# Kernel tuning notes

Hardware: AMD Instinct MI355X
Metric: run time of the kernel (lower is better)

Reference implementation:

```python
import jax, jax.numpy as jnp
import numpy as np

D_MODEL = 1024
HEADS = 8
WINDOW = 64
N_PATCH = 512
N_TOK = 512
TEXT_D = 768
IMAGE_D = 1024
B = 1


def _sliding_window_attn(x, ctx, qw, qb, kw, kb, vw, vb, ow, ob, window, heads):
    # Faithful to the torch loop: window i covers context[max(0,i-w//2) : min(T,i+w//2+1)+1],
    # i.e. up to w+2 real tokens; zero-padded (unmasked!) up to w tokens when shorter.
    B_, N, Dm = x.shape
    T = ctx.shape[1]
    L = window + 2
    dh = Dm // heads
    q = x @ qw.T + qb  # (B,N,D)
    idx = jnp.arange(N)[:, None] + (jnp.arange(L) - window // 2)[None, :]  # (N,L)
    valid = (idx >= 0) & (idx < T)                      # real context tokens
    length = valid.sum(-1)                              # real tokens per window
    n_zero = jnp.maximum(0, window - length)            # zero-pad count (torch pads to w)
    inv_rank = jnp.cumsum(~valid, axis=-1) - 1          # rank among invalid slots
    attend = valid | ((~valid) & (inv_rank < n_zero[:, None]))  # real + zero-pad slots
    ctxw = jnp.where(valid[None, :, :, None], ctx[:, jnp.clip(idx, 0, T - 1), :], 0.0)  # (B,N,L,D)
    k = ctxw @ kw.T + kb                                # bias hits zero-pad slots too (as torch)
    v = ctxw @ vw.T + vb
    qh = q.reshape(B_, N, heads, dh)
    kh = k.reshape(B_, N, L, heads, dh)
    vh = v.reshape(B_, N, L, heads, dh)
    s = jnp.einsum('bnhd,bnlhd->bhnl', qh, kh) / jnp.sqrt(jnp.asarray(dh, x.dtype))
    s = jnp.where(attend[None, None], s, jnp.asarray(-1e9, x.dtype))
    a = jax.nn.softmax(s, axis=-1)
    o = jnp.einsum('bhnl,bnlhd->bnhd', a, vh).reshape(B_, N, Dm)
    return o @ ow.T + ob + x  # residual add, as in torch loop


def setup_inputs() -> dict:
    key = jax.random.key(0)
    ks = jax.random.split(key, 32)
    s = 0.02
    inp = {
        'images': jax.random.normal(ks[0], (B, N_PATCH, IMAGE_D), jnp.float32),
        'capitions': jax.random.normal(ks[1], (B, N_TOK, TEXT_D), jnp.float32),
        'text_input_ids': jax.random.randint(ks[2], (B, N_TOK), 0, 32000, jnp.int64)
        if jax.config.jax_enable_x64 else jax.random.randint(ks[2], (B, N_TOK), 0, 32000, jnp.int32),
        'tp_w': jax.random.normal(ks[3], (D_MODEL, TEXT_D), jnp.float32) * s,
        'tp_b': jnp.zeros((D_MODEL,), jnp.float32),
        'ip_w': jax.random.normal(ks[4], (D_MODEL, IMAGE_D), jnp.float32) * s,
        'ip_b': jnp.zeros((D_MODEL,), jnp.float32),
    }
    names = ['qw', 'kw', 'vw', 'ow']
    i = 5
    for pre in ['ia_', 'ta_']:
        for n in names:
            inp[pre + n] = jax.random.normal(ks[i], (D_MODEL, D_MODEL), jnp.float32) * s
            inp[pre + n[0] + 'b'] = jnp.zeros((D_MODEL,), jnp.float32)
            i += 1
    return inp


def reference(images, capitions, text_input_ids,
              tp_w, tp_b, ip_w, ip_b,
              ia_qw, ia_qb, ia_kw, ia_kb, ia_vw, ia_vb, ia_ow, ia_ob,
              ta_qw, ta_qb, ta_kw, ta_kb, ta_vw, ta_vb, ta_ow, ta_ob):
    txt = capitions @ tp_w.T + tp_b   # (B,Ntok,D)
    img = images @ ip_w.T + ip_b      # (B,Npatch,D)
    fused_img = _sliding_window_attn(img, txt, ia_qw, ia_qb, ia_kw, ia_kb,
                                     ia_vw, ia_vb, ia_ow, ia_ob, WINDOW, HEADS)
    fused_txt = _sliding_window_attn(txt, img, ta_qw, ta_qb, ta_kw, ta_kb,
                                     ta_vw, ta_vb, ta_ow, ta_ob, WINDOW, HEADS)
    return fused_img, fused_txt
```

## Files before the change

kernel.cpp:

```cpp
#include <hip/hip_runtime.h>
#include <hip/hip_bf16.h>

#define MDIM 512
#define NDIM 1024
#define LSLOT 66

typedef __attribute__((ext_vector_type(8))) short short8;
typedef __attribute__((ext_vector_type(4))) short short4v;
typedef __attribute__((ext_vector_type(4))) float f32x4;
typedef __hip_bfloat16 bf16;

static __device__ __forceinline__ short f2bf(float f) {
    return __builtin_bit_cast(short, __float2bfloat16(f));
}
static __device__ __forceinline__ short8 cvt8(float4 a, float4 b) {
    short8 v;
    v[0] = f2bf(a.x); v[1] = f2bf(a.y); v[2] = f2bf(a.z); v[3] = f2bf(a.w);
    v[4] = f2bf(b.x); v[5] = f2bf(b.y); v[6] = f2bf(b.z); v[7] = f2bf(b.w);
    return v;
}

static __device__ __forceinline__ void gload16(const void* g, void* l) {
    __builtin_amdgcn_global_load_lds(
        (const __attribute__((address_space(1))) unsigned int*)g,
        (__attribute__((address_space(3))) unsigned int*)l, 16, 0, 0);
}

struct CvtDesc { const float* src; bf16* dst; int n; };
struct CvtBatch { CvtDesc d[12]; };

__global__ __launch_bounds__(256) void cvt_bf16(CvtBatch cb) {
    CvtDesc c = cb.d[blockIdx.z];
    const int i = (blockIdx.x * 256 + threadIdx.x) * 8;
    if (i >= c.n) return;
    const float4 a = *(const float4*)(c.src + i);
    const float4 b = *(const float4*)(c.src + i + 4);
    *(short8*)((short*)c.dst + i) = cvt8(a, b);
}

struct GDesc {
    const bf16* A;
    const bf16* W;
    const float* bias;
    const float* res;
    float* C;
    bf16* Cb;
    int K;
};
struct GBatch { GDesc d[6]; };

__global__ __launch_bounds__(128) void gemm_bf16(GBatch gb) {
    GDesc g = gb.d[blockIdx.z];
    const int K = g.K;
    __shared__ __align__(16) short lds[3][2][64 * 64];

    const int tid  = threadIdx.x;
    const int lane = tid & 63;
    const int wave = tid >> 6;
    const int m0 = blockIdx.y * 64;
    const int n0 = blockIdx.x * 64;
    const int wm = wave * 32;

    const size_t rowb = (size_t)K * 2;
    const char* sbase = (const char*)(wave ? (const void*)g.W : (const void*)g.A)
                      + (size_t)(wave ? n0 : m0) * rowb
                      + (size_t)(lane >> 3) * rowb
                      + (size_t)(((lane & 7) ^ (lane >> 3)) << 4);

    const int fr = lane & 15;
    const int fq = lane >> 4;

    f32x4 acc[2][4] = {};
    const int NT = K / 64;

#pragma unroll
    for (int tt = 0; tt < 3; ++tt)
#pragma unroll
        for (int i = 0; i < 8; ++i)
            gload16(sbase + (size_t)tt * 128 + (size_t)i * 8 * rowb,
                    &lds[tt][wave][i * 512]);

#define GSTEP(VMW)                                                              \
    {                                                                           \
        asm volatile("s_waitcnt vmcnt(" #VMW ")" ::: "memory");                 \
        __builtin_amdgcn_s_barrier();         \
        __builtin_amdgcn_sched_barrier(0);                                      \
        const int b = t % 3;                                                    \
        short8 af[2][2], wf[4][2];                                              \
        _Pragma("unroll")                                                       \
        for (int kk = 0; kk < 2; ++kk) {                                        \
            const int ch = kk * 4 + fq;                                         \
            _Pragma("unroll")                                                   \
            for (int i = 0; i < 2; ++i) {                                       \
                const int r = wm + i * 16 + fr;                                 \
                af[i][kk] = *(const short8*)&lds[b][0][r * 64 + ((ch ^ (r & 7)) << 3)]; \
            }                                                                   \
            _Pragma("unroll")                                                   \
            for (int j = 0; j < 4; ++j) {                                       \
                const int c = j * 16 + fr;                                      \
                wf[j][kk] = *(const short8*)&lds[b][1][c * 64 + ((ch ^ (c & 7)) << 3)]; \
            }                                                                   \
        }                                                                       \
        asm volatile("s_waitcnt lgkmcnt(0)" ::: "memory");                      \
        __builtin_amdgcn_sched_barrier(0);                                      \
        __builtin_amdgcn_s_barrier();              \
        if (t + 3 < NT) {                                                       \
            const char* p = sbase + (size_t)(t + 3) * 128;                      \
            _Pragma("unroll")                                                   \
            for (int i = 0; i < 8; ++i)                                         \
                gload16(p + (size_t)i * 8 * rowb, &lds[b][wave][i * 512]);      \
        }                                                                       \
        _Pragma("unroll")                                                       \
        for (int kk = 0; kk < 2; ++kk)                                          \
            _Pragma("unroll")                                                   \
            for (int i = 0; i < 2; ++i)                                         \
                _Pragma("unroll")                                               \
                for (int j = 0; j < 4; ++j)                                     \
                    acc[i][j] = __builtin_amdgcn_mfma_f32_16x16x32_bf16(        \
                        af[i][kk], wf[j][kk], acc[i][j], 0, 0, 0);              \
    }

    int t = 0;
    for (; t < NT - 2; ++t) GSTEP(16)
    GSTEP(8)
    ++t;
    GSTEP(0)
#undef GSTEP

#pragma unroll
    for (int i = 0; i < 2; ++i) {
        const int row0 = m0 + wm + i * 16 + fq * 4;
#pragma unroll
        for (int j = 0; j < 4; ++j) {
            const int col = n0 + j * 16 + fr;
            const float b = g.bias[col];
#pragma unroll
            for (int r = 0; r < 4; ++r) {
                float v = acc[i][j][r] + b;
                const size_t o = (size_t)(row0 + r) * NDIM + col;
                if (g.res) v += g.res[o];
                g.C[o] = v;
                if (g.Cb) g.Cb[o] = __float2bfloat16(v);
            }
        }
    }
}

struct AttnArgs {
    const float *Q, *K, *V, *kb, *vb;
    bf16* O;
};

__global__ __launch_bounds__(256) void attn_tile(AttnArgs a0, AttnArgs a1) {
    const AttnArgs a = blockIdx.z ? a1 : a0;
    const int h  = blockIdx.y;
    const int n0 = blockIdx.x * 32;
    const int tid = threadIdx.x;

    __shared__ float Ks[97 * 128];
    __shared__ float Vs[97 * 128];
    __shared__ float Qs[32 * 132];
    __shared__ float Ps[32 * 68];
    __shared__ float InvS[32];

    for (int i = tid; i < 97 * 32; i += 256) {
        const int wp = i >> 5, d4 = i & 31;
        const int idx = n0 - 32 + wp;
        const bool valid = (idx >= 0) && (idx < MDIM);
        const float* sk = (valid ? (a.K + (size_t)idx * NDIM) : a.kb) + h * 128;
        const float* sv = (valid ? (a.V + (size_t)idx * NDIM) : a.vb) + h * 128;
        const float4 kv = *(const float4*)(sk + d4 * 4);
        const float4 vv = *(const float4*)(sv + d4 * 4);
        const int slot = d4 ^ (wp & 31);
        *(float4*)&Ks[wp * 128 + slot * 4] = kv;
        *(float4*)&Vs[wp * 128 + slot * 4] = vv;
    }
    for (int i = tid; i < 32 * 32; i += 256) {
        const int r = i >> 5, d4 = i & 31;
        *(float4*)&Qs[r * 132 + d4 * 4] =
            *(const float4*)(a.Q + (size_t)(n0 + r) * NDIM + h * 128 + d4 * 4);
    }
    __syncthreads();

    const int r = tid >> 3, sub = tid & 7;
    const int n = n0 + r;
    const int lo_inv = max(0, 32 - n);
    const int hi_inv = max(0, n - 478);
    const int n_zero = max(0, 64 - (LSLOT - lo_inv - hi_inv));
    const float scale = 0.088388347648318447f;

    float dots[9];
#pragma unroll
    for (int k = 0; k < 9; ++k) dots[k] = 0.f;
#pragma unroll
    for (int db = 0; db < 4; ++db) {
        float4 q[8];
#pragma unroll
        for (int c = 0; c < 8; ++c) q[c] = *(float4*)&Qs[r * 132 + (db * 8 + c) * 4];
        for (int k = 0; k < 9; ++k) {
            const int l = sub + 8 * k;
            if (l >= LSLOT) break;
            const int wp = r + l, key = wp & 31;
            float accd = dots[k];
#pragma unroll
            for (int c = 0; c < 8; ++c) {
                const int d4 = db * 8 + c;
                const float4 kv = *(float4*)&Ks[wp * 128 + (d4 ^ key) * 4];
                accd += kv.x * q[c].x + kv.y * q[c].y + kv.z * q[c].z + kv.w * q[c].w;
            }
            dots[k] = accd;
        }
    }
    for (int k = 0; k < 9; ++k) {
        const int l = sub + 8 * k;
        if (l >= LSLOT) break;
        const int idx = n - 32 + l;
        const bool valid = (idx >= 0) && (idx < MDIM);
        bool attend = valid;
        if (!valid) {
            const int ir = (l < lo_inv) ? l : (l - (LSLOT - hi_inv));
            attend = ir < n_zero;
        }
        Ps[r * 68 + l] = attend ? dots[k] * scale : -1e30f;
    }
    __syncthreads();

    {
        float m = -1e30f;
        for (int k = 0; k < 9; ++k) {
            const int l = sub + 8 * k;
            if (l < LSLOT) m = fmaxf(m, Ps[r * 68 + l]);
        }
        for (int s = 1; s < 8; s <<= 1) m = fmaxf(m, __shfl_xor(m, s, 64));
        float sum = 0.f;
        for (int k = 0; k < 9; ++k) {
            const int l = sub + 8 * k;
            if (l >= LSLOT) break;
            const float e = expf(Ps[r * 68 + l] - m);
            Ps[r * 68 + l] = e;
            sum += e;
        }
        for (int s = 1; s < 8; s <<= 1) sum += __shfl_xor(sum, s, 64);
        if (sub == 0) InvS[r] = 1.0f / sum;
    }
    __syncthreads();

    float4 acc[4] = {};
    for (int l = 0; l < LSLOT; ++l) {
        const float p = Ps[r * 68 + l];
        const int wp = r + l, key = wp & 31;
#pragma unroll
        for (int c = 0; c < 4; ++c) {
            const int d4 = sub + 8 * c;
            const float4 vv = *(float4*)&Vs[wp * 128 + (d4 ^ key) * 4];
            acc[c].x += p * vv.x; acc[c].y += p * vv.y;
            acc[c].z += p * vv.z; acc[c].w += p * vv.w;
        }
    }
    const float inv = InvS[r];
#pragma unroll
    for (int c = 0; c < 4; ++c) {
        short4v o;
        o[0] = f2bf(acc[c].x * inv); o[1] = f2bf(acc[c].y * inv);
        o[2] = f2bf(acc[c].z * inv); o[3] = f2bf(acc[c].w * inv);
        *(short4v*)((short*)a.O + (size_t)n * NDIM + h * 128 + (sub + 8 * c) * 4) = o;
    }
}

extern "C" void kernel_launch(void* const* d_in, const int* in_sizes, int n_in,
                              void* d_out, int out_size, void* d_ws, size_t ws_size,
                              hipStream_t stream) {
    const float* images = (const float*)d_in[0];
    const float* caps   = (const float*)d_in[1];
    const float* tp_w = (const float*)d_in[3];
    const float* tp_b = (const float*)d_in[4];
    const float* ip_w = (const float*)d_in[5];
    const float* ip_b = (const float*)d_in[6];
    const float* ia_qw = (const float*)d_in[7];  const float* ia_qb = (const float*)d_in[8];
    const float* ia_kw = (const float*)d_in[9];  const float* ia_kb = (const float*)d_in[10];
    const float* ia_vw = (const float*)d_in[11]; const float* ia_vb = (const float*)d_in[12];
    const float* ia_ow = (const float*)d_in[13]; const float* ia_ob = (const float*)d_in[14];
    const float* ta_qw = (const float*)d_in[15]; const float* ta_qb = (const float*)d_in[16];
    const float* ta_kw = (const float*)d_in[17]; const float* ta_kb = (const float*)d_in[18];
    const float* ta_vw = (const float*)d_in[19]; const float* ta_vb = (const float*)d_in[20];
    const float* ta_ow = (const float*)d_in[21]; const float* ta_ob = (const float*)d_in[22];

    const size_t S = (size_t)MDIM * NDIM;
    float* ws = (float*)d_ws;
    float* txt = ws + 0 * S;
    float* img = ws + 1 * S;
    float* Qi  = ws + 2 * S;
    float* Ki  = ws + 3 * S;
    float* Vi  = ws + 4 * S;
    float* Qt  = ws + 5 * S;
    float* Kt  = ws + 6 * S;
    float* Vt  = ws + 7 * S;
    bf16* bb     = (bf16*)(ws + 8 * S);
    bf16* capsb  = bb;
    bf16* imgsb  = capsb + 393216;
    bf16* txtb   = imgsb + S;
    bf16* imgb   = txtb + S;
    bf16* Oib    = imgb + S;
    bf16* Otb    = Oib + S;
    bf16* tp_wb  = Otb + S;
    bf16* ip_wb  = tp_wb + 786432;
    bf16* qwb[8];
    { bf16* p = ip_wb + 1048576;
      for (int i = 0; i < 8; ++i) { qwb[i] = p; p += 1048576; } }

    float* fused_img = (float*)d_out;
    float* fused_txt = (float*)d_out + S;

    CvtBatch cv = {};
    cv.d[0]  = {caps,   capsb, 393216};
    cv.d[1]  = {images, imgsb, (int)S};
    cv.d[2]  = {tp_w,   tp_wb, 786432};
    cv.d[3]  = {ip_w,   ip_wb, 1048576};
    cv.d[4]  = {ia_qw, qwb[0], 1048576};
    cv.d[5]  = {ia_kw, qwb[1], 1048576};
    cv.d[6]  = {ia_vw, qwb[2], 1048576};
    cv.d[7]  = {ia_ow, qwb[3], 1048576};
    cv.d[8]  = {ta_qw, qwb[4], 1048576};
    cv.d[9]  = {ta_kw, qwb[5], 1048576};
    cv.d[10] = {ta_vw, qwb[6], 1048576};
    cv.d[11] = {ta_ow, qwb[7], 1048576};
    cvt_bf16<<<dim3(512, 1, 12), 256, 0, stream>>>(cv);

    dim3 blk(128);
    dim3 tiles(NDIM / 64, MDIM / 64);

    GBatch b1 = {};
    b1.d[0] = {capsb, tp_wb, tp_b, nullptr, txt, txtb, 768};
    b1.d[1] = {imgsb, ip_wb, ip_b, nullptr, img, imgb, 1024};
    gemm_bf16<<<dim3(tiles.x, tiles.y, 2), blk, 0, stream>>>(b1);

    GBatch b2 = {};
    b2.d[0] = {imgb, qwb[0], ia_qb, nullptr, Qi, nullptr, 1024};
    b2.d[1] = {txtb, qwb[1], ia_kb, nullptr, Ki, nullptr, 1024};
    b2.d[2] = {txtb, qwb[2], ia_vb, nullptr, Vi, nullptr, 1024};
    b2.d[3] = {txtb, qwb[4], ta_qb, nullptr, Qt, nullptr, 1024};
    b2.d[4] = {imgb, qwb[5], ta_kb, nullptr, Kt, nullptr, 1024};
    b2.d[5] = {imgb, qwb[6], ta_vb, nullptr, Vt, nullptr, 1024};
    gemm_bf16<<<dim3(tiles.x, tiles.y, 6), blk, 0, stream>>>(b2);

    AttnArgs aa = {Qi, Ki, Vi, ia_kb, ia_vb, Oib};
    AttnArgs ab = {Qt, Kt, Vt, ta_kb, ta_vb, Otb};
    attn_tile<<<dim3(16, 8, 2), 256, 0, stream>>>(aa, ab);

    GBatch b4 = {};
    b4.d[0] = {Oib, qwb[3], ia_ob, img, fused_img, nullptr, 1024};
    b4.d[1] = {Otb, qwb[7], ta_ob, txt, fused_txt, nullptr, 1024};
    gemm_bf16<<<dim3(tiles.x, tiles.y, 2), blk, 0, stream>>>(b4);
}
```

Before: 179.8 us.

## Fuse all stages into one persistent kernel with atomic grid barriers

Merges the bf16 conversion, the projection GEMMs, the QKV GEMMs, the attention and the output GEMM into a single 256-block kernel. Stages are separated by software grid barriers built on atomic counters, which are zeroed with a memset before each launch. Each block runs two GEMM tile units of two waves each, and the attention stage reuses the same shared memory. The aim is to remove four kernel launch gaps and tail effects. In exchange it relies on all 256 blocks being resident at once, uses large LDS per block, and leaves some blocks idle in stages with fewer tiles.

```diff
diff --git a/kernel.cpp b/kernel.cpp
--- a/kernel.cpp
+++ b/kernel.cpp
@@ -4,6 +4,7 @@
 #define MDIM 512
 #define NDIM 1024
 #define LSLOT 66
+#define NBLK 256u
 
 typedef __attribute__((ext_vector_type(8))) short short8;
 typedef __attribute__((ext_vector_type(4))) short short4v;
@@ -19,7 +20,6 @@
     v[4] = f2bf(b.x); v[5] = f2bf(b.y); v[6] = f2bf(b.z); v[7] = f2bf(b.w);
     return v;
 }
-
 static __device__ __forceinline__ void gload16(const void* g, void* l) {
     __builtin_amdgcn_global_load_lds(
         (const __attribute__((address_space(1))) unsigned int*)g,
@@ -27,17 +27,6 @@
 }
 
 struct CvtDesc { const float* src; bf16* dst; int n; };
-struct CvtBatch { CvtDesc d[12]; };
-
-__global__ __launch_bounds__(256) void cvt_bf16(CvtBatch cb) {
-    CvtDesc c = cb.d[blockIdx.z];
-    const int i = (blockIdx.x * 256 + threadIdx.x) * 8;
-    if (i >= c.n) return;
-    const float4 a = *(const float4*)(c.src + i);
-    const float4 b = *(const float4*)(c.src + i + 4);
-    *(short8*)((short*)c.dst + i) = cvt8(a, b);
-}
-
 struct GDesc {
     const bf16* A;
     const bf16* W;
@@ -47,28 +36,38 @@
     bf16* Cb;
     int K;
 };
-struct GBatch { GDesc d[6]; };
-
-__global__ __launch_bounds__(128) void gemm_bf16(GBatch gb) {
-    GDesc g = gb.d[blockIdx.z];
+struct AttnArgs { const float *Q, *K, *V, *kb, *vb; bf16* O; };
+struct FusedArgs {
+    CvtDesc cv[12];
+    GDesc s1[2], s2[6], s4[2];
+    AttnArgs at[2];
+    unsigned* bar;
+};
+
+static __device__ __forceinline__ void grid_bar(unsigned* ctr) {
+    __syncthreads();
+    if (threadIdx.x == 0) {
+        __threadfence();
+        __hip_atomic_fetch_add(ctr, 1u, __ATOMIC_ACQ_REL, __HIP_MEMORY_SCOPE_AGENT);
+        while (__hip_atomic_load(ctr, __ATOMIC_ACQUIRE, __HIP_MEMORY_SCOPE_AGENT) < NBLK)
+            __builtin_amdgcn_s_sleep(4);
+        __threadfence();
+    }
+    __syncthreads();
+}
+
+static __device__ void gemm_tile(const GDesc& g, int m0, int n0,
+                                 short* L, int w2, int lane) {
     const int K = g.K;
-    __shared__ __align__(16) short lds[3][2][64 * 64];
-
-    const int tid  = threadIdx.x;
-    const int lane = tid & 63;
-    const int wave = tid >> 6;
-    const int m0 = blockIdx.y * 64;
-    const int n0 = blockIdx.x * 64;
-    const int wm = wave * 32;
-
     const size_t rowb = (size_t)K * 2;
-    const char* sbase = (const char*)(wave ? (const void*)g.W : (const void*)g.A)
-                      + (size_t)(wave ? n0 : m0) * rowb
+    const char* sbase = (const char*)(w2 ? (const void*)g.W : (const void*)g.A)
+                      + (size_t)(w2 ? n0 : m0) * rowb
                       + (size_t)(lane >> 3) * rowb
                       + (size_t)(((lane & 7) ^ (lane >> 3)) << 4);
-
     const int fr = lane & 15;
     const int fq = lane >> 4;
+    const int wm = w2 * 32;
+    short* Lw = L + w2 * 4096;
 
     f32x4 acc[2][4] = {};
     const int NT = K / 64;
@@ -78,12 +77,12 @@
 #pragma unroll
         for (int i = 0; i < 8; ++i)
             gload16(sbase + (size_t)tt * 128 + (size_t)i * 8 * rowb,
-                    &lds[tt][wave][i * 512]);
+                    Lw + tt * 8192 + i * 512);
 
 #define GSTEP(VMW)                                                              \
     {                                                                           \
         asm volatile("s_waitcnt vmcnt(" #VMW ")" ::: "memory");                 \
-        __builtin_amdgcn_s_barrier();         \
+        __builtin_amdgcn_s_barrier();          \
         __builtin_amdgcn_sched_barrier(0);                                      \
         const int b = t % 3;                                                    \
         short8 af[2][2], wf[4][2];                                              \
@@ -93,12 +92,12 @@
             _Pragma("unroll")                                                   \
             for (int i = 0; i < 2; ++i) {                                       \
                 const int r = wm + i * 16 + fr;                                 \
-                af[i][kk] = *(const short8*)&lds[b][0][r * 64 + ((ch ^ (r & 7)) << 3)]; \
+                af[i][kk] = *(const short8*)&L[b * 8192 + r * 64 + ((ch ^ (r & 7)) << 3)]; \
             }                                                                   \
             _Pragma("unroll")                                                   \
             for (int j = 0; j < 4; ++j) {                                       \
                 const int c = j * 16 + fr;                                      \
-                wf[j][kk] = *(const short8*)&lds[b][1][c * 64 + ((ch ^ (c & 7)) << 3)]; \
+                wf[j][kk] = *(const short8*)&L[b * 8192 + 4096 + c * 64 + ((ch ^ (c & 7)) << 3)]; \
             }                                                                   \
         }                                                                       \
         asm volatile("s_waitcnt lgkmcnt(0)" ::: "memory");                      \
@@ -108,7 +107,7 @@
             const char* p = sbase + (size_t)(t + 3) * 128;                      \
             _Pragma("unroll")                                                   \
             for (int i = 0; i < 8; ++i)                                         \
-                gload16(p + (size_t)i * 8 * rowb, &lds[b][wave][i * 512]);      \
+                gload16(p + (size_t)i * 8 * rowb, Lw + b * 8192 + i * 512);     \
         }                                                                       \
         _Pragma("unroll")                                                       \
         for (int kk = 0; kk < 2; ++kk)                                          \
@@ -146,124 +145,173 @@
     }
 }
 
-struct AttnArgs {
-    const float *Q, *K, *V, *kb, *vb;
-    bf16* O;
-};
-
-__global__ __launch_bounds__(256) void attn_tile(AttnArgs a0, AttnArgs a1) {
-    const AttnArgs a = blockIdx.z ? a1 : a0;
-    const int h  = blockIdx.y;
-    const int n0 = blockIdx.x * 32;
-    const int tid = threadIdx.x;
-
-    __shared__ float Ks[97 * 128];
-    __shared__ float Vs[97 * 128];
-    __shared__ float Qs[32 * 132];
-    __shared__ float Ps[32 * 68];
-    __shared__ float InvS[32];
-
-    for (int i = tid; i < 97 * 32; i += 256) {
-        const int wp = i >> 5, d4 = i & 31;
-        const int idx = n0 - 32 + wp;
-        const bool valid = (idx >= 0) && (idx < MDIM);
-        const float* sk = (valid ? (a.K + (size_t)idx * NDIM) : a.kb) + h * 128;
-        const float* sv = (valid ? (a.V + (size_t)idx * NDIM) : a.vb) + h * 128;
-        const float4 kv = *(const float4*)(sk + d4 * 4);
-        const float4 vv = *(const float4*)(sv + d4 * 4);
-        const int slot = d4 ^ (wp & 31);
-        *(float4*)&Ks[wp * 128 + slot * 4] = kv;
-        *(float4*)&Vs[wp * 128 + slot * 4] = vv;
-    }
-    for (int i = tid; i < 32 * 32; i += 256) {
-        const int r = i >> 5, d4 = i & 31;
-        *(float4*)&Qs[r * 132 + d4 * 4] =
-            *(const float4*)(a.Q + (size_t)(n0 + r) * NDIM + h * 128 + d4 * 4);
-    }
-    __syncthreads();
-
-    const int r = tid >> 3, sub = tid & 7;
-    const int n = n0 + r;
-    const int lo_inv = max(0, 32 - n);
-    const int hi_inv = max(0, n - 478);
-    const int n_zero = max(0, 64 - (LSLOT - lo_inv - hi_inv));
-    const float scale = 0.088388347648318447f;
-
-    float dots[9];
-#pragma unroll
-    for (int k = 0; k < 9; ++k) dots[k] = 0.f;
-#pragma unroll
-    for (int db = 0; db < 4; ++db) {
-        float4 q[8];
-#pragma unroll
-        for (int c = 0; c < 8; ++c) q[c] = *(float4*)&Qs[r * 132 + (db * 8 + c) * 4];
+__global__ __launch_bounds__(256) void fused(FusedArgs fa) {
+    __shared__ __align__(16) char smem[125056];
+    const int tid  = threadIdx.x;
+    const int bi   = blockIdx.x;
+    const int lane = tid & 63;
+    const int wave = tid >> 6;
+    const int unit = wave >> 1;
+    const int w2   = wave & 1;
+
+    {
+        const int gtid = bi * 256 + tid;
+#pragma unroll 1
+        for (int d = 0; d < 12; ++d) {
+            const CvtDesc c = fa.cv[d];
+            for (int i = gtid * 8; i < c.n; i += 65536 * 8) {
+                const float4 a = *(const float4*)(c.src + i);
+                const float4 b = *(const float4*)(c.src + i + 4);
+                *(short8*)((short*)c.dst + i) = cvt8(a, b);
+            }
+        }
+    }
+    grid_bar(fa.bar + 0);
+
+    short* L = (short*)(smem + unit * 49152);
+
+    if (bi < 128) {
+        const int tile = bi * 2 + unit;
+        const GDesc& g = fa.s1[tile >> 7];
+        const int w = tile & 127;
+        gemm_tile(g, (w >> 4) * 64, (w & 15) * 64, L, w2, lane);
+    }
+    grid_bar(fa.bar + 1);
+
+    {
+        const int tile = bi * 2 + unit;
+        const GDesc& g = fa.s2[tile >> 7];
+        const int w = tile & 127;
+        gemm_tile(g, (w >> 4) * 64, (w & 15) * 64, L, w2, lane);
+    }
+    if (bi < 128) {
+        const int tile = 512 + bi * 2 + unit;
+        const GDesc& g = fa.s2[tile >> 7];
+        const int w = tile & 127;
+        gemm_tile(g, (w >> 4) * 64, (w & 15) * 64, L, w2, lane);
+    }
+    grid_bar(fa.bar + 2);
+
+    {
+        const AttnArgs a = (bi >= 128) ? fa.at[1] : fa.at[0];
+        const int h  = (bi >> 4) & 7;
+        const int n0 = (bi & 15) * 32;
+        float* Ks = (float*)smem;
+        float* Vs = Ks + 12416;
+        float* Qs = Vs + 12416;
+        float* Ps = Qs + 4224;
+        float* InvS = Ps + 2176;
+
+        for (int i = tid; i < 97 * 32; i += 256) {
+            const int wp = i >> 5, d4 = i & 31;
+            const int idx = n0 - 32 + wp;
+            const bool valid = (idx >= 0) && (idx < MDIM);
+            const float* sk = (valid ? (a.K + (size_t)idx * NDIM) : a.kb) + h * 128;
+            const float* sv = (valid ? (a.V + (size_t)idx * NDIM) : a.vb) + h * 128;
+            const float4 kv = *(const float4*)(sk + d4 * 4);
+            const float4 vv = *(const float4*)(sv + d4 * 4);
+            const int slot = d4 ^ (wp & 31);
+            *(float4*)&Ks[wp * 128 + slot * 4] = kv;
+            *(float4*)&Vs[wp * 128 + slot * 4] = vv;
+        }
+        for (int i = tid; i < 32 * 32; i += 256) {
+            const int r = i >> 5, d4 = i & 31;
+            *(float4*)&Qs[r * 132 + d4 * 4] =
+                *(const float4*)(a.Q + (size_t)(n0 + r) * NDIM + h * 128 + d4 * 4);
+        }
+        __syncthreads();
+
+        const int r = tid >> 3, sub = tid & 7;
+        const int n = n0 + r;
+        const int lo_inv = max(0, 32 - n);
+        const int hi_inv = max(0, n - 478);
+        const int n_zero = max(0, 64 - (LSLOT - lo_inv - hi_inv));
+        const float scale = 0.088388347648318447f;
+
+        float dots[9];
+#pragma unroll
+        for (int k = 0; k < 9; ++k) dots[k] = 0.f;
+#pragma unroll
+        for (int db = 0; db < 4; ++db) {
+            float4 q[8];
+#pragma unroll
+            for (int c = 0; c < 8; ++c) q[c] = *(float4*)&Qs[r * 132 + (db * 8 + c) * 4];
+            for (int k = 0; k < 9; ++k) {
+                const int l = sub + 8 * k;
+                if (l >= LSLOT) break;
+                const int wp = r + l, key = wp & 31;
+                float accd = dots[k];
+#pragma unroll
+                for (int c = 0; c < 8; ++c) {
+                    const int d4 = db * 8 + c;
+                    const float4 kv = *(float4*)&Ks[wp * 128 + (d4 ^ key) * 4];
+                    accd += kv.x * q[c].x + kv.y * q[c].y + kv.z * q[c].z + kv.w * q[c].w;
+                }
+                dots[k] = accd;
+            }
+        }
         for (int k = 0; k < 9; ++k) {
             const int l = sub + 8 * k;
             if (l >= LSLOT) break;
+            const int idx = n - 32 + l;
+            const bool valid = (idx >= 0) && (idx < MDIM);
+            bool attend = valid;
+            if (!valid) {
+                const int ir = (l < lo_inv) ? l : (l - (LSLOT - hi_inv));
+                attend = ir < n_zero;
+            }
+            Ps[r * 68 + l] = attend ? dots[k] * scale : -1e30f;
+        }
+        __syncthreads();
+
+        {
+            float m = -1e30f;
+            for (int k = 0; k < 9; ++k) {
+                const int l = sub + 8 * k;
+                if (l < LSLOT) m = fmaxf(m, Ps[r * 68 + l]);
+            }
+            for (int s = 1; s < 8; s <<= 1) m = fmaxf(m, __shfl_xor(m, s, 64));
+            float sum = 0.f;
+            for (int k = 0; k < 9; ++k) {
+                const int l = sub + 8 * k;
+                if (l >= LSLOT) break;
+                const float e = expf(Ps[r * 68 + l] - m);
+                Ps[r * 68 + l] = e;
+                sum += e;
+            }
+            for (int s = 1; s < 8; s <<= 1) sum += __shfl_xor(sum, s, 64);
+            if (sub == 0) InvS[r] = 1.0f / sum;
+        }
+        __syncthreads();
+
+        float4 acc[4] = {};
+        for (int l = 0; l < LSLOT; ++l) {
+            const float p = Ps[r * 68 + l];
             const int wp = r + l, key = wp & 31;
-            float accd = dots[k];
-#pragma unroll
-            for (int c = 0; c < 8; ++c) {
-                const int d4 = db * 8 + c;
-                const float4 kv = *(float4*)&Ks[wp * 128 + (d4 ^ key) * 4];
-                accd += kv.x * q[c].x + kv.y * q[c].y + kv.z * q[c].z + kv.w * q[c].w;
-            }
-            dots[k] = accd;
-        }
-    }
-    for (int k = 0; k < 9; ++k) {
-        const int l = sub + 8 * k;
-        if (l >= LSLOT) break;
-        const int idx = n - 32 + l;
-        const bool valid = (idx >= 0) && (idx < MDIM);
-        bool attend = valid;
-        if (!valid) {
-            const int ir = (l < lo_inv) ? l : (l - (LSLOT - hi_inv));
-            attend = ir < n_zero;
-        }
-        Ps[r * 68 + l] = attend ? dots[k] * scale : -1e30f;
-    }
-    __syncthreads();
-
-    {
-        float m = -1e30f;
-        for (int k = 0; k < 9; ++k) {
-            const int l = sub + 8 * k;
-            if (l < LSLOT) m = fmaxf(m, Ps[r * 68 + l]);
-        }
-        for (int s = 1; s < 8; s <<= 1) m = fmaxf(m, __shfl_xor(m, s, 64));
-        float sum = 0.f;
-        for (int k = 0; k < 9; ++k) {
-            const int l = sub + 8 * k;
-            if (l >= LSLOT) break;
-            const float e = expf(Ps[r * 68 + l] - m);
-            Ps[r * 68 + l] = e;
-            sum += e;
-        }
-        for (int s = 1; s < 8; s <<= 1) sum += __shfl_xor(sum, s, 64);
-        if (sub == 0) InvS[r] = 1.0f / sum;
-    }
-    __syncthreads();
-
-    float4 acc[4] = {};
-    for (int l = 0; l < LSLOT; ++l) {
-        const float p = Ps[r * 68 + l];
-        const int wp = r + l, key = wp & 31;
+#pragma unroll
+            for (int c = 0; c < 4; ++c) {
+                const int d4 = sub + 8 * c;
+                const float4 vv = *(float4*)&Vs[wp * 128 + (d4 ^ key) * 4];
+                acc[c].x += p * vv.x; acc[c].y += p * vv.y;
+                acc[c].z += p * vv.z; acc[c].w += p * vv.w;
+            }
+        }
+        const float inv = InvS[r];
 #pragma unroll
         for (int c = 0; c < 4; ++c) {
-            const int d4 = sub + 8 * c;
-            const float4 vv = *(float4*)&Vs[wp * 128 + (d4 ^ key) * 4];
-            acc[c].x += p * vv.x; acc[c].y += p * vv.y;
-            acc[c].z += p * vv.z; acc[c].w += p * vv.w;
-        }
-    }
-    const float inv = InvS[r];
-#pragma unroll
-    for (int c = 0; c < 4; ++c) {
-        short4v o;
-        o[0] = f2bf(acc[c].x * inv); o[1] = f2bf(acc[c].y * inv);
-        o[2] = f2bf(acc[c].z * inv); o[3] = f2bf(acc[c].w * inv);
-        *(short4v*)((short*)a.O + (size_t)n * NDIM + h * 128 + (sub + 8 * c) * 4) = o;
+            short4v o;
+            o[0] = f2bf(acc[c].x * inv); o[1] = f2bf(acc[c].y * inv);
+            o[2] = f2bf(acc[c].z * inv); o[3] = f2bf(acc[c].w * inv);
+            *(short4v*)((short*)a.O + (size_t)n * NDIM + h * 128 + (sub + 8 * c) * 4) = o;
+        }
+    }
+    grid_bar(fa.bar + 3);
+
+    if (bi < 128) {
+        const int tile = bi * 2 + unit;
+        const GDesc& g = fa.s4[tile >> 7];
+        const int w = tile & 127;
+        gemm_tile(g, (w >> 4) * 64, (w & 15) * 64, L, w2, lane);
     }
 }
 
@@ -311,44 +359,40 @@
     float* fused_img = (float*)d_out;
     float* fused_txt = (float*)d_out + S;
 
-    CvtBatch cv = {};
-    cv.d[0]  = {caps,   capsb, 393216};
-    cv.d[1]  = {images, imgsb, (int)S};
-    cv.d[2]  = {tp_w,   tp_wb, 786432};
-    cv.d[3]  = {ip_w,   ip_wb, 1048576};
-    cv.d[4]  = {ia_qw, qwb[0], 1048576};
-    cv.d[5]  = {ia_kw, qwb[1], 1048576};
-    cv.d[6]  = {ia_vw, qwb[2], 1048576};
-    cv.d[7]  = {ia_ow, qwb[3], 1048576};
-    cv.d[8]  = {ta_qw, qwb[4], 1048576};
-    cv.d[9]  = {ta_kw, qwb[5], 1048576};
-    cv.d[10] = {ta_vw, qwb[6], 1048576};
-    cv.d[11] = {ta_ow, qwb[7], 1048576};
-    cvt_bf16<<<dim3(512, 1, 12), 256, 0, stream>>>(cv);
-
-    dim3 blk(128);
-    dim3 tiles(NDIM / 64, MDIM / 64);
-
-    GBatch b1 = {};
-    b1.d[0] = {capsb, tp_wb, tp_b, nullptr, txt, txtb, 768};
-    b1.d[1] = {imgsb, ip_wb, ip_b, nullptr, img, imgb, 1024};
-    gemm_bf16<<<dim3(tiles.x, tiles.y, 2), blk, 0, stream>>>(b1);
-
-    GBatch b2 = {};
-    b2.d[0] = {imgb, qwb[0], ia_qb, nullptr, Qi, nullptr, 1024};
-    b2.d[1] = {txtb, qwb[1], ia_kb, nullptr, Ki, nullptr, 1024};
-    b2.d[2] = {txtb, qwb[2], ia_vb, nullptr, Vi, nullptr, 1024};
-    b2.d[3] = {txtb, qwb[4], ta_qb, nullptr, Qt, nullptr, 1024};
-    b2.d[4] = {imgb, qwb[5], ta_kb, nullptr, Kt, nullptr, 1024};
-    b2.d[5] = {imgb, qwb[6], ta_vb, nullptr, Vt, nullptr, 1024};
-    gemm_bf16<<<dim3(tiles.x, tiles.y, 6), blk, 0, stream>>>(b2);
-
-    AttnArgs aa = {Qi, Ki, Vi, ia_kb, ia_vb, Oib};
-    AttnArgs ab = {Qt, Kt, Vt, ta_kb, ta_vb, Otb};
-    attn_tile<<<dim3(16, 8, 2), 256, 0, stream>>>(aa, ab);
-
-    GBatch b4 = {};
-    b4.d[0] = {Oib, qwb[3], ia_ob, img, fused_img, nullptr, 1024};
-    b4.d[1] = {Otb, qwb[7], ta_ob, txt, fused_txt, nullptr, 1024};
-    gemm_bf16<<<dim3(tiles.x, tiles.y, 2), blk, 0, stream>>>(b4);
-}
+    unsigned* bar = (unsigned*)((char*)d_ws + (64u << 20));
+
+    FusedArgs fa = {};
+    fa.cv[0]  = {caps,   capsb, 393216};
+    fa.cv[1]  = {images, imgsb, (int)S};
+    fa.cv[2]  = {tp_w,   tp_wb, 786432};
+    fa.cv[3]  = {ip_w,   ip_wb, 1048576};
+    fa.cv[4]  = {ia_qw, qwb[0], 1048576};
+    fa.cv[5]  = {ia_kw, qwb[1], 1048576};
+    fa.cv[6]  = {ia_vw, qwb[2], 1048576};
+    fa.cv[7]  = {ia_ow, qwb[3], 1048576};
+    fa.cv[8]  = {ta_qw, qwb[4], 1048576};
+    fa.cv[9]  = {ta_kw, qwb[5], 1048576};
+    fa.cv[10] = {ta_vw, qwb[6], 1048576};
+    fa.cv[11] = {ta_ow, qwb[7], 1048576};
+
+    fa.s1[0] = {capsb, tp_wb, tp_b, nullptr, txt, txtb, 768};
+    fa.s1[1] = {imgsb, ip_wb, ip_b, nullptr, img, imgb, 1024};
+
+    fa.s2[0] = {imgb, qwb[0], ia_qb, nullptr, Qi, nullptr, 1024};
+    fa.s2[1] = {txtb, qwb[1], ia_kb, nullptr, Ki, nullptr, 1024};
+    fa.s2[2] = {txtb, qwb[2], ia_vb, nullptr, Vi, nullptr, 1024};
+    fa.s2[3] = {txtb, qwb[4], ta_qb, nullptr, Qt, nullptr, 1024};
+    fa.s2[4] = {imgb, qwb[5], ta_kb, nullptr, Kt, nullptr, 1024};
+    fa.s2[5] = {imgb, qwb[6], ta_vb, nullptr, Vt, nullptr, 1024};
+
+    fa.at[0] = {Qi, Ki, Vi, ia_kb, ia_vb, Oib};
+    fa.at[1] = {Qt, Kt, Vt, ta_kb, ta_vb, Otb};
+
+    fa.s4[0] = {Oib, qwb[3], ia_ob, img, fused_img, nullptr, 1024};
+    fa.s4[1] = {Otb, qwb[7], ta_ob, txt, fused_txt, nullptr, 1024};
+
+    fa.bar = bar;
+
+    hipMemsetAsync(bar, 0, 64, stream);
+    fused<<<dim3(NBLK), dim3(256), 0, stream>>>(fa);
+}
```

Measured after the change: 524.1 us. 2.91x slower.

## Enlarge GEMM tiles to 128x128 with four waves and double buffering

Applied to the files above, without the earlier changes.

Reworks the batched bf16 GEMM from 64x64 tiles with two waves and triple-buffered LDS to 128x128 tiles with four waves, each computing a 64x64 sub-tile, and double-buffered LDS. The goal is more operand reuse per LDS load and fewer global loads per output. The cost is far fewer blocks: 32 per matrix, so 64 or 192 per launch on a GPU with many CUs. That risks under-occupancy, and the shallower prefetch exposes more memory latency.

```diff
diff --git a/kernel.cpp b/kernel.cpp
--- a/kernel.cpp
+++ b/kernel.cpp
@@ -19,7 +19,6 @@
     v[4] = f2bf(b.x); v[5] = f2bf(b.y); v[6] = f2bf(b.z); v[7] = f2bf(b.w);
     return v;
 }
-
 static __device__ __forceinline__ void gload16(const void* g, void* l) {
     __builtin_amdgcn_global_load_lds(
         (const __attribute__((address_space(1))) unsigned int*)g,
@@ -49,94 +48,94 @@
 };
 struct GBatch { GDesc d[6]; };
 
-__global__ __launch_bounds__(128) void gemm_bf16(GBatch gb) {
-    GDesc g = gb.d[blockIdx.z];
+__global__ __launch_bounds__(256, 2) void gemm_bf16(GBatch gb) {
+    GDesc g = gb.d[blockIdx.y];
     const int K = g.K;
-    __shared__ __align__(16) short lds[3][2][64 * 64];
+    __shared__ __align__(16) char smem[65536];
 
     const int tid  = threadIdx.x;
     const int lane = tid & 63;
     const int wave = tid >> 6;
-    const int m0 = blockIdx.y * 64;
-    const int n0 = blockIdx.x * 64;
-    const int wm = wave * 32;
-
+    const int wr = wave >> 1, wc = wave & 1;
+    const int tile = blockIdx.x;
+    const int m0 = (tile >> 3) * 128;
+    const int n0 = (tile & 7) * 128;
+
+    const int isW  = wave >> 1;
+    const int half = wave & 1;
     const size_t rowb = (size_t)K * 2;
-    const char* sbase = (const char*)(wave ? (const void*)g.W : (const void*)g.A)
-                      + (size_t)(wave ? n0 : m0) * rowb
-                      + (size_t)(lane >> 3) * rowb
+    const char* sbase = (const char*)(isW ? (const void*)g.W : (const void*)g.A)
+                      + (size_t)((isW ? n0 : m0) + half * 64 + (lane >> 3)) * rowb
                       + (size_t)(((lane & 7) ^ (lane >> 3)) << 4);
+    const int dbase = isW * 16384 + half * 8192 + lane * 16;
 
     const int fr = lane & 15;
     const int fq = lane >> 4;
 
-    f32x4 acc[2][4] = {};
+    f32x4 acc[4][4] = {};
     const int NT = K / 64;
 
 #pragma unroll
-    for (int tt = 0; tt < 3; ++tt)
+    for (int tt = 0; tt < 2; ++tt)
 #pragma unroll
         for (int i = 0; i < 8; ++i)
             gload16(sbase + (size_t)tt * 128 + (size_t)i * 8 * rowb,
-                    &lds[tt][wave][i * 512]);
+                    smem + tt * 32768 + dbase + i * 1024);
 
 #define GSTEP(VMW)                                                              \
     {                                                                           \
         asm volatile("s_waitcnt vmcnt(" #VMW ")" ::: "memory");                 \
-        __builtin_amdgcn_s_barrier();         \
+        __builtin_amdgcn_s_barrier();          \
         __builtin_amdgcn_sched_barrier(0);                                      \
-        const int b = t % 3;                                                    \
-        short8 af[2][2], wf[4][2];                                              \
+        const char* Lb = smem + (t & 1) * 32768;                                \
+        short8 af[4][2], wf[4][2];                                              \
         _Pragma("unroll")                                                       \
         for (int kk = 0; kk < 2; ++kk) {                                        \
             const int ch = kk * 4 + fq;                                         \
+            const int sw = (ch ^ (fr & 7)) << 4;                                \
             _Pragma("unroll")                                                   \
-            for (int i = 0; i < 2; ++i) {                                       \
-                const int r = wm + i * 16 + fr;                                 \
-                af[i][kk] = *(const short8*)&lds[b][0][r * 64 + ((ch ^ (r & 7)) << 3)]; \
-            }                                                                   \
-            _Pragma("unroll")                                                   \
-            for (int j = 0; j < 4; ++j) {                                       \
-                const int c = j * 16 + fr;                                      \
-                wf[j][kk] = *(const short8*)&lds[b][1][c * 64 + ((ch ^ (c & 7)) << 3)]; \
+            for (int fi = 0; fi < 4; ++fi) {                                    \
+                const int ra = wr * 64 + fi * 16 + fr;                          \
+                af[fi][kk] = *(const short8*)(Lb + ra * 128 + sw);              \
+                const int rw = wc * 64 + fi * 16 + fr;                          \
+                wf[fi][kk] = *(const short8*)(Lb + 16384 + rw * 128 + sw);      \
             }                                                                   \
         }                                                                       \
         asm volatile("s_waitcnt lgkmcnt(0)" ::: "memory");                      \
         __builtin_amdgcn_sched_barrier(0);                                      \
-        __builtin_amdgcn_s_barrier();              \
-        if (t + 3 < NT) {                                                       \
-            const char* p = sbase + (size_t)(t + 3) * 128;                      \
+        __builtin_amdgcn_s_barrier();                \
+        if (t + 2 < NT) {                                                       \
+            const char* p = sbase + (size_t)(t + 2) * 128;                      \
+            char* d = smem + (t & 1) * 32768 + dbase;                           \
             _Pragma("unroll")                                                   \
             for (int i = 0; i < 8; ++i)                                         \
-                gload16(p + (size_t)i * 8 * rowb, &lds[b][wave][i * 512]);      \
+                gload16(p + (size_t)i * 8 * rowb, d + i * 1024);                \
         }                                                                       \
         _Pragma("unroll")                                                       \
         for (int kk = 0; kk < 2; ++kk)                                          \
             _Pragma("unroll")                                                   \
-            for (int i = 0; i < 2; ++i)                                         \
+            for (int fi = 0; fi < 4; ++fi)                                      \
                 _Pragma("unroll")                                               \
-                for (int j = 0; j < 4; ++j)                                     \
-                    acc[i][j] = __builtin_amdgcn_mfma_f32_16x16x32_bf16(        \
-                        af[i][kk], wf[j][kk], acc[i][j], 0, 0, 0);              \
+                for (int fj = 0; fj < 4; ++fj)                                  \
+                    acc[fi][fj] = __builtin_amdgcn_mfma_f32_16x16x32_bf16(      \
+                        af[fi][kk], wf[fj][kk], acc[fi][fj], 0, 0, 0);          \
     }
 
     int t = 0;
-    for (; t < NT - 2; ++t) GSTEP(16)
-    GSTEP(8)
-    ++t;
+    for (; t < NT - 1; ++t) GSTEP(8)
     GSTEP(0)
 #undef GSTEP
 
 #pragma unroll
-    for (int i = 0; i < 2; ++i) {
-        const int row0 = m0 + wm + i * 16 + fq * 4;
-#pragma unroll
-        for (int j = 0; j < 4; ++j) {
-            const int col = n0 + j * 16 + fr;
+    for (int fi = 0; fi < 4; ++fi) {
+        const int row0 = m0 + wr * 64 + fi * 16 + fq * 4;
+#pragma unroll
+        for (int fj = 0; fj < 4; ++fj) {
+            const int col = n0 + wc * 64 + fj * 16 + fr;
             const float b = g.bias[col];
 #pragma unroll
             for (int r = 0; r < 4; ++r) {
-                float v = acc[i][j][r] + b;
+                float v = acc[fi][fj][r] + b;
                 const size_t o = (size_t)(row0 + r) * NDIM + col;
                 if (g.res) v += g.res[o];
                 g.C[o] = v;
@@ -326,13 +325,12 @@
     cv.d[11] = {ta_ow, qwb[7], 1048576};
     cvt_bf16<<<dim3(512, 1, 12), 256, 0, stream>>>(cv);
 
-    dim3 blk(128);
-    dim3 tiles(NDIM / 64, MDIM / 64);
+    dim3 blk(256);
 
     GBatch b1 = {};
     b1.d[0] = {capsb, tp_wb, tp_b, nullptr, txt, txtb, 768};
     b1.d[1] = {imgsb, ip_wb, ip_b, nullptr, img, imgb, 1024};
-    gemm_bf16<<<dim3(tiles.x, tiles.y, 2), blk, 0, stream>>>(b1);
+    gemm_bf16<<<dim3(32, 2), blk, 0, stream>>>(b1);
 
     GBatch b2 = {};
     b2.d[0] = {imgb, qwb[0], ia_qb, nullptr, Qi, nullptr, 1024};
@@ -341,7 +339,7 @@
     b2.d[3] = {txtb, qwb[4], ta_qb, nullptr, Qt, nullptr, 1024};
     b2.d[4] = {imgb, qwb[5], ta_kb, nullptr, Kt, nullptr, 1024};
     b2.d[5] = {imgb, qwb[6], ta_vb, nullptr, Vt, nullptr, 1024};
-    gemm_bf16<<<dim3(tiles.x, tiles.y, 6), blk, 0, stream>>>(b2);
+    gemm_bf16<<<dim3(32, 6), blk, 0, stream>>>(b2);
 
     AttnArgs aa = {Qi, Ki, Vi, ia_kb, ia_vb, Oib};
     AttnArgs ab = {Qt, Kt, Vt, ta_kb, ta_vb, Otb};
@@ -350,5 +348,5 @@
     GBatch b4 = {};
     b4.d[0] = {Oib, qwb[3], ia_ob, img, fused_img, nullptr, 1024};
     b4.d[1] = {Otb, qwb[7], ta_ob, txt, fused_txt, nullptr, 1024};
-    gemm_bf16<<<dim3(tiles.x, tiles.y, 2), blk, 0, stream>>>(b4);
-}
+    gemm_bf16<<<dim3(32, 2), blk, 0, stream>>>(b4);
+}
```

Result: slower. 206.2 us (+14.7%).
